# Performance work log

Measured on AMD Instinct MI355X. Metric: run time of the kernel, lower is better.

The kernel has to match this reference:

```python
import jax, jax.numpy as jnp
import numpy as np
import math

FACTOR = 5  # self.factor


def setup_inputs() -> dict:
    key = jax.random.key(0)
    kq, kk, kv = jax.random.split(key, 3)
    B, L, H, D = 4, 2048, 8, 64
    return {
        "queries": jax.random.normal(kq, (B, L, H, D), dtype=jnp.float32),
        "keys": jax.random.normal(kk, (B, L, H, D), dtype=jnp.float32),
        "values": jax.random.normal(kv, (B, L, H, D), dtype=jnp.float32),
        "attn_mask": jnp.zeros((1,), dtype=jnp.int32),  # unused by the module's forward
    }


def _prob_attention(queries, keys, values):
    B, L_Q, H, D = queries.shape
    L_K = keys.shape[1]
    # to (B, H, L, D)
    Q = queries.transpose(0, 2, 1, 3)
    K = keys.transpose(0, 2, 1, 3)
    V = values.transpose(0, 2, 1, 3)

    U_part = min(FACTOR * int(math.ceil(math.log(L_K))), L_K)  # sample_k
    u = min(FACTOR * int(math.ceil(math.log(L_Q))), L_Q)       # n_top

    # --- _prob_QE: sampled QK, sparsity measure M, top-u query selection ---
    idx_key = jax.random.key(42)  # fixed key stands in for torch.randint
    index_sample = jax.random.randint(idx_key, (L_Q, U_part), 0, L_K)  # [L_Q, S]
    K_sample = K[:, :, index_sample, :]                                # [B,H,L_Q,S,E]
    Q_K_sample = jnp.einsum('bhqe,bhqse->bhqs', Q, K_sample)           # [B,H,L_Q,S]
    M = Q_K_sample.max(axis=-1) - Q_K_sample.sum(axis=-1) / L_K        # [B,H,L_Q]
    M_top = jax.lax.top_k(M, u)[1]                                     # [B,H,u]

    Q_reduce = jnp.take_along_axis(Q, M_top[..., None], axis=2)        # [B,H,u,E]
    scores = jnp.einsum('bhue,bhke->bhuk', Q_reduce, K)                # [B,H,u,L_K]
    scores = scores * (1.0 / math.sqrt(D))                             # scale=None -> 1/sqrt(D)

    # --- initial context (mask_flag=True path): mean of V over keys ---
    context = jnp.broadcast_to(V.mean(axis=2, keepdims=True), (B, H, L_Q, D))

    attn = jax.nn.softmax(scores, axis=-1)
    context_update = jnp.einsum('bhuk,bhkd->bhud', attn, V)            # [B,H,u,D]

    # scatter the updated rows back at the selected query positions
    b = jnp.arange(B)[:, None, None]
    h = jnp.arange(H)[None, :, None]
    context = context.at[b, h, M_top].set(context_update)

    return context.transpose(0, 2, 1, 3)  # [B, L_Q, H, D]


def reference(queries, keys, values, attn_mask):
    # attn_mask is accepted but unused by the torch module's mask_flag=True path
    return _prob_attention(queries, keys, values)
```

## Files before the change

kernel.cpp:

```cpp
#include <hip/hip_runtime.h>
#include <stdint.h>


static constexpr int Bc = 4, Lc = 2048, Hc = 8, Dc = 64, NUc = 40;
static constexpr int NCH = 32, CHK = 64;
static constexpr int UT = 10;

struct TF2 { uint32_t a, b; };

__host__ __device__ constexpr uint32_t rotl32c(uint32_t x, int r) {
    return (x << r) | (x >> (32 - r));
}

__host__ __device__ constexpr TF2 tf2x32c(uint32_t k0, uint32_t k1, uint32_t x0, uint32_t x1) {
    uint32_t ks[3] = {k0, k1, k0 ^ k1 ^ 0x1BD11BDAu};
    const int R0[4] = {13, 15, 26, 6};
    const int R1[4] = {17, 29, 16, 24};
    x0 += ks[0];
    x1 += ks[1];
    for (int i = 0; i < 5; ++i) {
        const int* R = (i & 1) ? R1 : R0;
        for (int j = 0; j < 4; ++j) {
            x0 += x1;
            x1 = rotl32c(x1, R[j]);
            x1 ^= x0;
        }
        x0 += ks[(i + 1) % 3];
        x1 += ks[(i + 2) % 3] + (uint32_t)(i + 1);
    }
    return TF2{x0, x1};
}

__global__ __launch_bounds__(256, 4) void k_M(const float* __restrict__ Q,
                                              const float* __restrict__ K,
                                              float* __restrict__ M,
                                              float* __restrict__ vm) {
    constexpr TF2 K2 = tf2x32c(0u, 42u, 0u, 1u);
    int lane = threadIdx.x & 63;
    int w = threadIdx.x >> 6;
    int blk = blockIdx.x;
    if (blk < 8) vm[blk * 256 + threadIdx.x] = 0.f;
    int xcd = blk & 7;
    int local = blk >> 3;
    int b = xcd >> 1;
    int q = (xcd & 1) * 1024 + local * 4 + w;
    int h = lane >> 3;
    int myidx = 0;
    if (lane < 40) {
        TF2 r = tf2x32c(K2.a, K2.b, 0u, (uint32_t)(q * 40 + lane));
        myidx = (int)((r.a ^ r.b) & 2047u);
    }

    const float4* Q4 = reinterpret_cast<const float4*>(Q);
    const float4* K4 = reinterpret_cast<const float4*>(K);
    size_t qb = (size_t)(b * Lc + q) * 128;
    float4 qv0 = Q4[qb + 2 * lane];
    float4 qv1 = Q4[qb + 2 * lane + 1];

    float mx8[8], sm8[8];
#pragma unroll
    for (int j = 0; j < 8; ++j) { mx8[j] = -INFINITY; sm8[j] = 0.f; }
#pragma unroll
    for (int i = 0; i < 5; ++i) {
#pragma unroll
        for (int j = 0; j < 8; ++j) {
            int kk = __shfl(myidx, i * 8 + j, 64);
            size_t rb = (size_t)(b * Lc + kk) * 128;
            float4 kv0 = K4[rb + 2 * lane];
            float4 kv1 = K4[rb + 2 * lane + 1];
            float pv = qv0.x * kv0.x + qv0.y * kv0.y + qv0.z * kv0.z + qv0.w * kv0.w +
                       qv1.x * kv1.x + qv1.y * kv1.y + qv1.z * kv1.z + qv1.w * kv1.w;
#pragma unroll
            for (int m = 1; m < 8; m <<= 1) pv += __shfl_xor(pv, m, 64);
            mx8[j] = fmaxf(mx8[j], pv);
            sm8[j] += pv;
        }
    }
    float mx = mx8[0], sm = sm8[0];
#pragma unroll
    for (int j = 1; j < 8; ++j) { mx = fmaxf(mx, mx8[j]); sm += sm8[j]; }
    if ((lane & 7) == 0) M[(b * 8 + h) * Lc + q] = mx - sm * (1.0f / 2048.0f);
}

__global__ __launch_bounds__(256) void k_topk(const float* __restrict__ M, int* __restrict__ top,
                                              uint32_t* __restrict__ gmask) {
    __shared__ uint32_t hist[256];
    __shared__ uint32_t sh_bin, sh_need;
    __shared__ int sel[NUc];
    __shared__ int tie[128];
    __shared__ uint32_t selCnt, tieCnt;
    int bh = blockIdx.x;
    int t = threadIdx.x;
    uint32_t uk[8];
#pragma unroll
    for (int i = 0; i < 8; ++i) {
        uint32_t s = __float_as_uint(M[bh * Lc + i * 256 + t]);
        uk[i] = (s & 0x80000000u) ? ~s : (s | 0x80000000u);
    }
    uint32_t prefix = 0, need = NUc;
    for (int pass = 0; pass < 4; ++pass) {
        int shift = 24 - 8 * pass;
        hist[t] = 0;
        __syncthreads();
#pragma unroll
        for (int i = 0; i < 8; ++i) {
            bool ok = (pass == 0) || ((uk[i] >> (shift + 8)) == prefix);
            if (ok) atomicAdd(&hist[(uk[i] >> shift) & 255u], 1u);
        }
        __syncthreads();
        if (t < 64) {
            uint32_t c0 = hist[4 * t], c1 = hist[4 * t + 1];
            uint32_t c2 = hist[4 * t + 2], c3 = hist[4 * t + 3];
            uint32_t s = c0 + c1 + c2 + c3;
            uint32_t suf = s;
#pragma unroll
            for (int m = 1; m < 64; m <<= 1) {
                uint32_t o = __shfl_down(suf, m, 64);
                if (t + m < 64) suf += o;
            }
            uint32_t above = suf - s;
            if (suf >= need && above < need) {
                uint32_t rem = need - above;
                uint32_t bsel, cnt;
                if (c3 >= rem) { bsel = 4 * t + 3; cnt = rem; }
                else if (c3 + c2 >= rem) { bsel = 4 * t + 2; cnt = rem - c3; }
                else if (c3 + c2 + c1 >= rem) { bsel = 4 * t + 1; cnt = rem - c3 - c2; }
                else { bsel = 4 * t; cnt = rem - c3 - c2 - c1; }
                sh_bin = bsel;
                sh_need = cnt;
            }
        }
        __syncthreads();
        prefix = (pass == 0) ? sh_bin : ((prefix << 8) | sh_bin);
        need = sh_need;
        __syncthreads();
    }
    const uint32_t T = prefix;
    if (t == 0) { selCnt = 0; tieCnt = 0; }
    __syncthreads();
#pragma unroll
    for (int i = 0; i < 8; ++i) {
        int idx = i * 256 + t;
        if (uk[i] > T) {
            uint32_t slot = atomicAdd(&selCnt, 1u);
            if (slot < NUc) sel[slot] = idx;
        } else if (uk[i] == T) {
            uint32_t slot = atomicAdd(&tieCnt, 1u);
            if (slot < 128) tie[slot] = idx;
        }
    }
    __syncthreads();
    if (t == 0) {
        int n = (int)tieCnt;
        if (n > 128) n = 128;
        for (int a = 1; a < n; ++a) {
            int key = tie[a], c = a - 1;
            while (c >= 0 && tie[c] > key) { tie[c + 1] = tie[c]; --c; }
            tie[c + 1] = key;
        }
        uint32_t base = selCnt;
        for (uint32_t j = 0; j < need && base + j < NUc; ++j) sel[base + j] = tie[j];
    }
    __syncthreads();
    if (t < NUc) top[bh * NUc + t] = sel[t];
    if (t < 64) {
        uint32_t word = 0;
#pragma unroll
        for (int j = 0; j < NUc; ++j) {
            int s = sel[j];
            if ((s >> 5) == t) word |= 1u << (s & 31);
        }
        gmask[bh * 64 + t] = word;
    }
}

__global__ __launch_bounds__(256, 4) void k_attn_part(const float* __restrict__ Q,
                                                      const float* __restrict__ K,
                                                      const float* __restrict__ V,
                                                      const int* __restrict__ top,
                                                      float* __restrict__ wsO,
                                                      float* __restrict__ wsm,
                                                      float* __restrict__ wsl,
                                                      float* __restrict__ vm) {
    __shared__ float Qs[40][64];
    __shared__ float Ks[64][68];
    __shared__ float pT[4][64][12];
    __shared__ int tqs[40];
    int blk = blockIdx.x;
    int xcd = blk & 7, local = blk >> 3;
    int bh = xcd * 4 + (local >> 5);
    int chunk = local & 31;
    int b = bh >> 3, h = bh & 7;
    int t = threadIdx.x, w = t >> 6, lane = t & 63;

    if (t < 40) tqs[t] = top[bh * NUc + t];
    __syncthreads();
    for (int i = t; i < 40 * 64; i += 256) {
        int u = i >> 6, d = i & 63;
        Qs[u][d] = Q[(((size_t)(b * Lc + tqs[u])) * Hc + h) * Dc + d];
    }
    const float* Kbase = K + (((size_t)(b * Lc + chunk * CHK)) * Hc + h) * Dc;
    for (int f = t; f < 1024; f += 256) {
        int r = f >> 4, c = f & 15;
        *reinterpret_cast<float4*>(&Ks[r][c * 4]) =
            *reinterpret_cast<const float4*>(Kbase + (size_t)r * 512 + c * 4);
    }
    __syncthreads();

    float acc[UT];
#pragma unroll
    for (int u = 0; u < UT; ++u) acc[u] = 0.f;
#pragma unroll
    for (int i = 0; i < 16; ++i) {
        float4 kv = *reinterpret_cast<const float4*>(&Ks[lane][i * 4]);
#pragma unroll
        for (int u = 0; u < UT; ++u) {
            float4 qv = *reinterpret_cast<const float4*>(&Qs[w * UT + u][i * 4]);
            acc[u] += qv.x * kv.x + qv.y * kv.y + qv.z * kv.z + qv.w * kv.w;
        }
    }
#pragma unroll
    for (int u = 0; u < UT; ++u) acc[u] *= 0.125f;
    float mr[UT];
#pragma unroll
    for (int u = 0; u < UT; ++u) {
        float v = acc[u];
#pragma unroll
        for (int m = 1; m < 64; m <<= 1) v = fmaxf(v, __shfl_xor(v, m, 64));
        mr[u] = v;
    }
    float pr[UT];
#pragma unroll
    for (int u = 0; u < UT; ++u) {
        pr[u] = __expf(acc[u] - mr[u]);
        pT[w][lane][u] = pr[u];
    }
    float sr[UT];
#pragma unroll
    for (int u = 0; u < UT; ++u) {
        float v = pr[u];
#pragma unroll
        for (int m = 1; m < 64; m <<= 1) v += __shfl_xor(v, m, 64);
        sr[u] = v;
    }
    int sbase = (bh * NCH + chunk) * NUc + w * UT;
#pragma unroll
    for (int u = 0; u < UT; ++u) {
        if (lane == u) {
            wsm[sbase + u] = mr[u];
            wsl[sbase + u] = sr[u];
        }
    }
#pragma unroll
    for (int u = 0; u < UT; ++u) acc[u] = 0.f;
    float vs = 0.f;
    const float* Vbh = V + ((size_t)b * Lc * Hc + h) * Dc;
    for (int k = 0; k < 64; ++k) {
        float vv = Vbh[(size_t)(chunk * CHK + k) * 512 + lane];
        vs += vv;
        float4 pa = *reinterpret_cast<const float4*>(&pT[w][k][0]);
        float4 pb = *reinterpret_cast<const float4*>(&pT[w][k][4]);
        float2 pc = *reinterpret_cast<const float2*>(&pT[w][k][8]);
        acc[0] += pa.x * vv; acc[1] += pa.y * vv; acc[2] += pa.z * vv; acc[3] += pa.w * vv;
        acc[4] += pb.x * vv; acc[5] += pb.y * vv; acc[6] += pb.z * vv; acc[7] += pb.w * vv;
        acc[8] += pc.x * vv; acc[9] += pc.y * vv;
    }
    if (w == 0) atomicAdd(&vm[bh * 64 + lane], vs * (1.0f / 2048.0f));
    size_t obase = (size_t)(bh * NCH + chunk) * 2560 + (size_t)(w * UT) * 64;
#pragma unroll
    for (int u = 0; u < UT; ++u) wsO[obase + u * 64 + lane] = acc[u];
}

__global__ void k_out_inl(const float* __restrict__ wsO, const float* __restrict__ wsm,
                          const float* __restrict__ wsl, const float* __restrict__ vm,
                          const int* __restrict__ top, const uint32_t* __restrict__ gmask,
                          float* __restrict__ out) {
    int o4 = blockIdx.x * blockDim.x + threadIdx.x;
    if (o4 >= Bc * Lc * Hc * (Dc / 4)) return;
    int dq = o4 & 15;
    int h = (o4 >> 4) & 7;
    int bl = o4 >> 7;
    int b = bl >> 11, l = bl & 2047;
    int bh = b * 8 + h;
    float4 v;
    uint32_t wmask = gmask[bh * 64 + (l >> 5)];
    if ((wmask >> (l & 31)) & 1u) {
        int u = 0;
#pragma unroll
        for (int j = 0; j < NUc; ++j)
            if (top[bh * NUc + j] == l) u = j;
        float cf[NCH];
        float m = -INFINITY;
#pragma unroll
        for (int c = 0; c < NCH; ++c) {
            cf[c] = wsm[(bh * NCH + c) * NUc + u];
            m = fmaxf(m, cf[c]);
        }
        float L = 0.f;
#pragma unroll
        for (int c = 0; c < NCH; ++c) {
            float e = __expf(cf[c] - m);
            L += wsl[(bh * NCH + c) * NUc + u] * e;
            cf[c] = e;
        }
        const float4* W4 = reinterpret_cast<const float4*>(wsO);
        float4 a = make_float4(0.f, 0.f, 0.f, 0.f);
#pragma unroll
        for (int c = 0; c < NCH; ++c) {
            float4 o = W4[(size_t)(bh * NCH + c) * 640 + u * 16 + dq];
            a.x += o.x * cf[c]; a.y += o.y * cf[c]; a.z += o.z * cf[c]; a.w += o.w * cf[c];
        }
        float inv = 1.0f / L;
        v = make_float4(a.x * inv, a.y * inv, a.z * inv, a.w * inv);
    } else {
        v = reinterpret_cast<const float4*>(vm)[bh * 16 + dq];
    }
    reinterpret_cast<float4*>(out)[o4] = v;
}

__global__ __launch_bounds__(256) void k_comb(const float* __restrict__ wsO,
                                              const float* __restrict__ wsm,
                                              const float* __restrict__ wsl,
                                              float* __restrict__ stage) {
    __shared__ float cm[NCH][5], cl[NCH][5], cf[NCH][5];
    int blk = blockIdx.x;
    int ut = blk & 7, bh = blk >> 3;
    int t = threadIdx.x;
    for (int i = t; i < NCH * 5; i += 256) {
        int c = i / 5, j = i % 5;
        cm[c][j] = wsm[(bh * NCH + c) * NUc + ut * 5 + j];
        cl[c][j] = wsl[(bh * NCH + c) * NUc + ut * 5 + j];
    }
    __syncthreads();
    if (t < 5) {
        float m = -INFINITY;
#pragma unroll
        for (int c = 0; c < NCH; ++c) m = fmaxf(m, cm[c][t]);
        float L = 0.f;
#pragma unroll
        for (int c = 0; c < NCH; ++c) {
            float f = __expf(cm[c][t] - m);
            L += cl[c][t] * f;
            cf[c][t] = f;
        }
        float inv = 1.0f / L;
#pragma unroll
        for (int c = 0; c < NCH; ++c) cf[c][t] *= inv;
    }
    __syncthreads();
    for (int i = t; i < 5 * 64; i += 256) {
        int j = i >> 6, d = i & 63;
        float val = 0.f;
#pragma unroll
        for (int c = 0; c < NCH; ++c)
            val += wsO[((size_t)(bh * NCH + c)) * 2560 + (ut * 5 + j) * 64 + d] * cf[c][j];
        stage[(size_t)bh * 2560 + (ut * 5 + j) * 64 + d] = val;
    }
}

__global__ void k_out(const float* __restrict__ stage, const float* __restrict__ vm,
                      const int* __restrict__ top, const uint32_t* __restrict__ gmask,
                      float* __restrict__ out) {
    int o4 = blockIdx.x * blockDim.x + threadIdx.x;
    if (o4 >= Bc * Lc * Hc * (Dc / 4)) return;
    int dq = o4 & 15;
    int h = (o4 >> 4) & 7;
    int bl = o4 >> 7;
    int b = bl >> 11, l = bl & 2047;
    int bh = b * 8 + h;
    float4 v;
    uint32_t wmask = gmask[bh * 64 + (l >> 5)];
    if ((wmask >> (l & 31)) & 1u) {
        int u = 0;
#pragma unroll
        for (int j = 0; j < NUc; ++j)
            if (top[bh * NUc + j] == l) u = j;
        v = reinterpret_cast<const float4*>(stage)[(bh * NUc + u) * 16 + dq];
    } else {
        v = reinterpret_cast<const float4*>(vm)[bh * 16 + dq];
    }
    reinterpret_cast<float4*>(out)[o4] = v;
}

extern "C" void kernel_launch(void* const* d_in, const int* in_sizes, int n_in,
                              void* d_out, int out_size, void* d_ws, size_t ws_size,
                              hipStream_t stream) {
    (void)in_sizes; (void)n_in; (void)out_size;
    const float* Q = (const float*)d_in[0];
    const float* K = (const float*)d_in[1];
    const float* V = (const float*)d_in[2];
    float* out = (float*)d_out;

    int*      top   = (int*)d_ws;
    float*    vm    = (float*)((char*)d_ws + 8192);
    uint32_t* gmask = (uint32_t*)((char*)d_ws + 16384);
    float* M = (float*)((char*)d_out + 11075584);

    const bool bigws = ws_size >= 11534336;

    if (bigws) {
        float* wsm = (float*)((char*)d_ws + 32768);
        float* wsl = (float*)((char*)d_ws + 196608);
        float* wsO = (float*)((char*)d_ws + 393216);
        hipLaunchKernelGGL(k_M, dim3(2048), dim3(256), 0, stream, Q, K, M, vm);
        hipLaunchKernelGGL(k_topk, dim3(Bc * Hc), dim3(256), 0, stream, M, top, gmask);
        hipLaunchKernelGGL(k_attn_part, dim3(1024), dim3(256), 0, stream, Q, K, V, top,
                           wsO, wsm, wsl, vm);
        hipLaunchKernelGGL(k_out_inl, dim3(4096), dim3(256), 0, stream, wsO, wsm, wsl, vm,
                           top, gmask, out);
    } else {
        float* wsO   = (float*)d_out;
        float* wsm   = (float*)((char*)d_out + 10485760);
        float* wsl   = (float*)((char*)d_out + 10649600);
        float* stage = (float*)((char*)d_ws + 24576);
        hipLaunchKernelGGL(k_M, dim3(2048), dim3(256), 0, stream, Q, K, M, vm);
        hipLaunchKernelGGL(k_topk, dim3(Bc * Hc), dim3(256), 0, stream, M, top, gmask);
        hipLaunchKernelGGL(k_attn_part, dim3(1024), dim3(256), 0, stream, Q, K, V, top,
                           wsO, wsm, wsl, vm);
        hipLaunchKernelGGL(k_comb, dim3(Bc * Hc * 8), dim3(256), 0, stream, wsO, wsm, wsl,
                           stage);
        hipLaunchKernelGGL(k_out, dim3(4096), dim3(256), 0, stream, stage, vm, top, gmask,
                           out);
    }
}
```

Before: 90.72 us.

## Split sampled-key scoring by key half per XCD and merge partial stats in top-k

The sparsity-measure kernel now runs twice as many blocks. Each XCD pair handles every query but only the sampled keys from one half of the sequence, so each XCD's L2 holds half of K's rows. Partial max and sum values go to four stat planes, and the top-k kernel merges them into M. Out-of-half samples are redirected to a fixed dummy row and masked out, so every block still issues all 40 loads. The cost is extra Q loads, doubled launch work and wasted dummy loads. An unroll pragma is also added to the attention V loop.

```diff
diff --git a/kernel.cpp b/kernel.cpp
--- a/kernel.cpp
+++ b/kernel.cpp
@@ -5,6 +5,7 @@
 static constexpr int Bc = 4, Lc = 2048, Hc = 8, Dc = 64, NUc = 40;
 static constexpr int NCH = 32, CHK = 64;
 static constexpr int UT = 10;
+static constexpr int SPLANE = 65536;
 
 struct TF2 { uint32_t a, b; };
 
@@ -33,7 +34,7 @@
 
 __global__ __launch_bounds__(256, 4) void k_M(const float* __restrict__ Q,
                                               const float* __restrict__ K,
-                                              float* __restrict__ M,
+                                              float* __restrict__ stat,
                                               float* __restrict__ vm) {
     constexpr TF2 K2 = tf2x32c(0u, 42u, 0u, 1u);
     int lane = threadIdx.x & 63;
@@ -41,9 +42,9 @@
     int blk = blockIdx.x;
     if (blk < 8) vm[blk * 256 + threadIdx.x] = 0.f;
     int xcd = blk & 7;
+    int b = xcd >> 1, half = xcd & 1;
     int local = blk >> 3;
-    int b = xcd >> 1;
-    int q = (xcd & 1) * 1024 + local * 4 + w;
+    int q = local * 4 + w;
     int h = lane >> 3;
     int myidx = 0;
     if (lane < 40) {
@@ -56,6 +57,7 @@
     size_t qb = (size_t)(b * Lc + q) * 128;
     float4 qv0 = Q4[qb + 2 * lane];
     float4 qv1 = Q4[qb + 2 * lane + 1];
+    const int dummy = half << 10;
 
     float mx8[8], sm8[8];
 #pragma unroll
@@ -65,24 +67,31 @@
 #pragma unroll
         for (int j = 0; j < 8; ++j) {
             int kk = __shfl(myidx, i * 8 + j, 64);
-            size_t rb = (size_t)(b * Lc + kk) * 128;
+            bool live = (kk >> 10) == half;
+            int kr = live ? kk : dummy;
+            size_t rb = (size_t)(b * Lc + kr) * 128;
             float4 kv0 = K4[rb + 2 * lane];
             float4 kv1 = K4[rb + 2 * lane + 1];
             float pv = qv0.x * kv0.x + qv0.y * kv0.y + qv0.z * kv0.z + qv0.w * kv0.w +
                        qv1.x * kv1.x + qv1.y * kv1.y + qv1.z * kv1.z + qv1.w * kv1.w;
 #pragma unroll
             for (int m = 1; m < 8; m <<= 1) pv += __shfl_xor(pv, m, 64);
-            mx8[j] = fmaxf(mx8[j], pv);
-            sm8[j] += pv;
+            mx8[j] = live ? fmaxf(mx8[j], pv) : mx8[j];
+            sm8[j] += live ? pv : 0.f;
         }
     }
     float mx = mx8[0], sm = sm8[0];
 #pragma unroll
     for (int j = 1; j < 8; ++j) { mx = fmaxf(mx, mx8[j]); sm += sm8[j]; }
-    if ((lane & 7) == 0) M[(b * 8 + h) * Lc + q] = mx - sm * (1.0f / 2048.0f);
-}
-
-__global__ __launch_bounds__(256) void k_topk(const float* __restrict__ M, int* __restrict__ top,
+    if ((lane & 7) == 0) {
+        int base = (b * 8 + h) * Lc + q;
+        stat[(half * 2 + 0) * SPLANE + base] = mx;
+        stat[(half * 2 + 1) * SPLANE + base] = sm;
+    }
+}
+
+__global__ __launch_bounds__(256) void k_topk(const float* __restrict__ stat,
+                                              int* __restrict__ top,
                                               uint32_t* __restrict__ gmask) {
     __shared__ uint32_t hist[256];
     __shared__ uint32_t sh_bin, sh_need;
@@ -94,7 +103,11 @@
     uint32_t uk[8];
 #pragma unroll
     for (int i = 0; i < 8; ++i) {
-        uint32_t s = __float_as_uint(M[bh * Lc + i * 256 + t]);
+        int base = bh * Lc + i * 256 + t;
+        float mx = fmaxf(stat[0 * SPLANE + base], stat[2 * SPLANE + base]);
+        float sm = stat[1 * SPLANE + base] + stat[3 * SPLANE + base];
+        float Mv = mx - sm * (1.0f / 2048.0f);
+        uint32_t s = __float_as_uint(Mv);
         uk[i] = (s & 0x80000000u) ? ~s : (s | 0x80000000u);
     }
     uint32_t prefix = 0, need = NUc;
@@ -255,6 +268,7 @@
     for (int u = 0; u < UT; ++u) acc[u] = 0.f;
     float vs = 0.f;
     const float* Vbh = V + ((size_t)b * Lc * Hc + h) * Dc;
+#pragma unroll 8
     for (int k = 0; k < 64; ++k) {
         float vv = Vbh[(size_t)(chunk * CHK + k) * 512 + lane];
         vs += vv;
@@ -394,7 +408,7 @@
     int*      top   = (int*)d_ws;
     float*    vm    = (float*)((char*)d_ws + 8192);
     uint32_t* gmask = (uint32_t*)((char*)d_ws + 16384);
-    float* M = (float*)((char*)d_out + 11075584);
+    float* stat = (float*)((char*)d_out + 11337728);
 
     const bool bigws = ws_size >= 11534336;
 
@@ -402,8 +416,8 @@
         float* wsm = (float*)((char*)d_ws + 32768);
         float* wsl = (float*)((char*)d_ws + 196608);
         float* wsO = (float*)((char*)d_ws + 393216);
-        hipLaunchKernelGGL(k_M, dim3(2048), dim3(256), 0, stream, Q, K, M, vm);
-        hipLaunchKernelGGL(k_topk, dim3(Bc * Hc), dim3(256), 0, stream, M, top, gmask);
+        hipLaunchKernelGGL(k_M, dim3(4096), dim3(256), 0, stream, Q, K, stat, vm);
+        hipLaunchKernelGGL(k_topk, dim3(Bc * Hc), dim3(256), 0, stream, stat, top, gmask);
         hipLaunchKernelGGL(k_attn_part, dim3(1024), dim3(256), 0, stream, Q, K, V, top,
                            wsO, wsm, wsl, vm);
         hipLaunchKernelGGL(k_out_inl, dim3(4096), dim3(256), 0, stream, wsO, wsm, wsl, vm,
@@ -413,8 +427,8 @@
         float* wsm   = (float*)((char*)d_out + 10485760);
         float* wsl   = (float*)((char*)d_out + 10649600);
         float* stage = (float*)((char*)d_ws + 24576);
-        hipLaunchKernelGGL(k_M, dim3(2048), dim3(256), 0, stream, Q, K, M, vm);
-        hipLaunchKernelGGL(k_topk, dim3(Bc * Hc), dim3(256), 0, stream, M, top, gmask);
+        hipLaunchKernelGGL(k_M, dim3(4096), dim3(256), 0, stream, Q, K, stat, vm);
+        hipLaunchKernelGGL(k_topk, dim3(Bc * Hc), dim3(256), 0, stream, stat, top, gmask);
         hipLaunchKernelGGL(k_attn_part, dim3(1024), dim3(256), 0, stream, Q, K, V, top,
                            wsO, wsm, wsl, vm);
         hipLaunchKernelGGL(k_comb, dim3(Bc * Hc * 8), dim3(256), 0, stream, wsO, wsm, wsl,
```

Measured after the change: 104.9 us. +15.6%, slower.
